# Performance work log

Hardware: AMD Instinct MI355X
Metric: run time of the kernel (lower is better)

## Reference

```python
import jax, jax.numpy as jnp
import numpy as np

EMBED_DIM = 1024
NUM_HEADS = 16
HEAD_DIM = EMBED_DIM // NUM_HEADS
ROPE_BASE = 10000.0


def rotate_half(x):
    d = x.shape[-1] // 2
    x1, x2 = x[..., :d], x[..., d:]
    return jnp.concatenate((-x2, x1), axis=-1)


def setup_inputs() -> dict:
    key = jax.random.key(0)
    k_x, k_wqkv, k_bqkv, k_wo, k_bo = jax.random.split(key, 5)
    C = EMBED_DIM
    x = jax.random.normal(k_x, (4, 2048, C), dtype=jnp.float32)
    s = 1.0 / np.sqrt(C)
    W_qkv = jax.random.uniform(k_wqkv, (C, 3 * C), minval=-s, maxval=s, dtype=jnp.float32)
    b_qkv = jax.random.uniform(k_bqkv, (3 * C,), minval=-s, maxval=s, dtype=jnp.float32)
    W_out = jax.random.uniform(k_wo, (C, C), minval=-s, maxval=s, dtype=jnp.float32)
    b_out = jax.random.uniform(k_bo, (C,), minval=-s, maxval=s, dtype=jnp.float32)
    return {"x": x, "W_qkv": W_qkv, "b_qkv": b_qkv, "W_out": W_out, "b_out": b_out}


def reference(x, W_qkv, b_qkv, W_out, b_out):
    B, T, C = x.shape
    H, Dh = NUM_HEADS, HEAD_DIM
    # fused QKV projection: [B,T,3C] -> [3,B,H,T,Dh]
    qkv = (x @ W_qkv + b_qkv).reshape(B, T, 3, H, Dh).transpose(2, 0, 3, 1, 4)
    q, k, v = qkv[0], qkv[1], qkv[2]
    # rotary embedding: freqs [T, Dh/2] -> emb [T, Dh]
    inv_freq = 1.0 / (ROPE_BASE ** (jnp.arange(0, Dh, 2, dtype=jnp.float32) / Dh))
    freqs = jnp.arange(T, dtype=jnp.float32)[:, None] * inv_freq[None, :]
    emb = jnp.concatenate((freqs, freqs), axis=-1)  # [T, Dh], broadcasts over B,H
    cos, sin = jnp.cos(emb), jnp.sin(emb)
    q = q * cos + rotate_half(q) * sin
    k = k * cos + rotate_half(k) * sin
    # full (non-causal) attention, manual softmax
    scale = 1.0 / np.sqrt(Dh)
    attn = jax.nn.softmax(jnp.einsum("bhqd,bhkd->bhqk", q, k) * scale, axis=-1)
    out = jnp.einsum("bhqk,bhkd->bhqd", attn, v)  # [B,H,T,Dh]
    out = out.transpose(0, 2, 1, 3).reshape(B, T, C)
    return out @ W_out + b_out
```

## Files before the change

kernel.cpp:

```cpp
#include <hip/hip_runtime.h>
#include <math.h>

#define T_SEQ 2048
#define CDIM  1024
#define NH    16
#define DHD   64
#define BATCH 4
#define MROWS (BATCH * T_SEQ)
#define BHN   (BATCH * NH)

typedef _Float16 f16;
typedef __attribute__((ext_vector_type(8))) _Float16 f16x8;
typedef __attribute__((ext_vector_type(4))) _Float16 f16x4;
typedef __attribute__((ext_vector_type(4))) float f32x4;

__device__ __forceinline__ void gl_lds16(const f16* g, f16* l) {
    __builtin_amdgcn_global_load_lds(
        (const __attribute__((address_space(1))) void*)(g),
        (__attribute__((address_space(3))) void*)(l),
        16, 0, 0);
}

__global__ void rope_tables_kernel(float* __restrict__ ctab, float* __restrict__ stab)
{
    int idx = blockIdx.x * 256 + threadIdx.x;
    int t = idx >> 5, i = idx & 31;
    double inv = pow(10000.0, -(double)(2 * i) / 64.0);
    double a = (double)t * inv;
    ctab[idx] = (float)cos(a);
    stab[idx] = (float)sin(a);
}

__global__ __launch_bounds__(256) void xcvt_kernel(
    const float* __restrict__ X, f16* __restrict__ Xf)
{
    int idx = blockIdx.x * 256 + threadIdx.x;
    const float4* src = (const float4*)X + (size_t)idx * 2;
    float4 a = src[0], b = src[1];
    f16x8 o;
    o[0] = (f16)a.x; o[1] = (f16)a.y; o[2] = (f16)a.z; o[3] = (f16)a.w;
    o[4] = (f16)b.x; o[5] = (f16)b.y; o[6] = (f16)b.z; o[7] = (f16)b.w;
    *((f16x8*)Xf + idx) = o;
}

__global__ __launch_bounds__(64) void wcvt_kernel(
    const float* __restrict__ W, f16* __restrict__ Wt, int N)
{
    int lane = threadIdx.x;
    int k0 = blockIdx.x * 8;
    int n = blockIdx.y * 64 + lane;
    f16x8 o;
#pragma unroll
    for (int j = 0; j < 8; j++) o[j] = (f16)W[(size_t)(k0 + j) * N + n];
    *(f16x8*)(Wt + (size_t)n * CDIM + k0) = o;
}

#define GEMM_MAINLOOP(Aimg, Bimg, M0, N0)                                         \
    __shared__ f16 As[128][32], Bs[128][32];                                      \
    const int tid = threadIdx.x, wave = tid >> 6, lane = tid & 63;                \
    const int l16 = lane & 15, quad = lane >> 4;                                  \
    const int wm = wave >> 1, wn = wave & 1;                                      \
    f32x4 acc[4][4];                                                              \
    _Pragma("unroll") for (int i = 0; i < 4; i++)                                 \
        _Pragma("unroll") for (int j = 0; j < 4; j++)                             \
            acc[i][j] = (f32x4){0.f, 0.f, 0.f, 0.f};                              \
    const f16* sbase = (wave < 2) ? (Aimg) : (Bimg);                              \
    f16* lbase = ((wave < 2) ? &As[0][0] : &Bs[0][0]) + (wave & 1) * 2048;        \
    const size_t srow0 = ((wave < 2) ? (size_t)(M0) : (size_t)(N0)) + (wave & 1) * 64; \
    const int srow = lane >> 2, schunk = (lane & 3) << 3;                         \
    for (int k0 = 0; k0 < CDIM; k0 += 32) {                                       \
        _Pragma("unroll") for (int it = 0; it < 4; it++)                          \
            gl_lds16(sbase + (srow0 + it * 16 + srow) * CDIM + k0 + schunk,       \
                     lbase + it * 512);                                           \
        __syncthreads();                                                          \
        f16x8 fa[4], fb[4];                                                       \
        _Pragma("unroll") for (int mi = 0; mi < 4; mi++)                          \
            fa[mi] = *(const f16x8*)&As[wm * 64 + mi * 16 + l16][quad * 8];       \
        _Pragma("unroll") for (int ni = 0; ni < 4; ni++)                          \
            fb[ni] = *(const f16x8*)&Bs[wn * 64 + ni * 16 + l16][quad * 8];       \
        _Pragma("unroll") for (int mi = 0; mi < 4; mi++)                          \
            _Pragma("unroll") for (int ni = 0; ni < 4; ni++)                      \
                acc[mi][ni] = __builtin_amdgcn_mfma_f32_16x16x32_f16(             \
                    fa[mi], fb[ni], acc[mi][ni], 0, 0, 0);                        \
        __syncthreads();                                                          \
    }

__global__ __launch_bounds__(256) void qkv_gemm_kernel(
    const f16* __restrict__ Xf, const f16* __restrict__ Wt,
    const float* __restrict__ bias,
    const float* __restrict__ ctab, const float* __restrict__ stab,
    f16* __restrict__ qf, f16* __restrict__ kf, f16* __restrict__ vf)
{
    const int m0 = blockIdx.x * 128;
    const int n0 = blockIdx.y * 128;
    GEMM_MAINLOOP(Xf, Wt, m0, n0)

    const int ncol0 = n0 + wn * 64;
    const int w = ncol0 >> 10;
    const int h = (ncol0 >> 6) & 15;
    const int b = m0 >> 11;
    const int trow0 = (m0 & 2047) + wm * 64 + quad * 4;
    float bia[4];
#pragma unroll
    for (int ni = 0; ni < 4; ni++) bia[ni] = bias[ncol0 + ni * 16 + l16];

    if (w < 2) {
        f16* oq = w ? kf : qf;
        const float sc = w ? 1.0f : 0.125f;
#pragma unroll
        for (int mi = 0; mi < 4; mi++) {
#pragma unroll
            for (int i = 0; i < 4; i++) {
                int t = trow0 + mi * 16 + i;
                size_t rowoff = ((size_t)(b * NH + h) * T_SEQ + t) * DHD;
#pragma unroll
                for (int np = 0; np < 2; np++) {
                    int d = np * 16 + l16;
                    float v0 = acc[mi][np][i] + bia[np];
                    float v1 = acc[mi][np + 2][i] + bia[np + 2];
                    float c = ctab[(t << 5) + d];
                    float s = stab[(t << 5) + d];
                    oq[rowoff + d]      = (f16)((v0 * c - v1 * s) * sc);
                    oq[rowoff + d + 32] = (f16)((v1 * c + v0 * s) * sc);
                }
            }
        }
    } else {
#pragma unroll
        for (int mi = 0; mi < 4; mi++) {
#pragma unroll
            for (int i = 0; i < 4; i++) {
                int t = trow0 + mi * 16 + i;
                size_t rowoff = ((size_t)(b * NH + h) * T_SEQ + t) * DHD;
#pragma unroll
                for (int ni = 0; ni < 4; ni++)
                    vf[rowoff + ni * 16 + l16] = (f16)(acc[mi][ni][i] + bia[ni]);
            }
        }
    }
}

__global__ __launch_bounds__(256) void vt_kernel(
    const f16* __restrict__ vf, f16* __restrict__ vt)
{
    __shared__ f16 Ls[64][72];
    const int tid = threadIdx.x;
    const int tb = blockIdx.x;
    const int bh = blockIdx.y;
#pragma unroll
    for (int p = 0; p < 2; p++) {
        int idx = tid + p * 256;
        int r = idx >> 3, c8 = (idx & 7) << 3;
        *(f16x8*)&Ls[r][c8] =
            *(const f16x8*)(vf + ((size_t)bh * T_SEQ + tb * 64 + r) * DHD + c8);
    }
    __syncthreads();
#pragma unroll
    for (int p = 0; p < 2; p++) {
        int idx = tid + p * 256;
        int d = idx >> 3, t8 = (idx & 7) << 3;
        f16x8 o;
#pragma unroll
        for (int j = 0; j < 8; j++) o[j] = Ls[t8 + j][d];
        *(f16x8*)(vt + ((size_t)bh * DHD + d) * T_SEQ + (size_t)tb * 64 + t8) = o;
    }
}

__global__ __launch_bounds__(256, 2) void attn_kernel(
    const f16* __restrict__ qf, const f16* __restrict__ kf,
    const f16* __restrict__ vt, f16* __restrict__ ab)
{
    __shared__ f16 Kb[2][64][72];
    __shared__ f16 Vb[2][64][72];
    __shared__ f16 Pb[4][64][40];
    __shared__ float Lb[4][64];

    const int tid  = threadIdx.x;
    const int wave = tid >> 6, lane = tid & 63;
    const int l16  = lane & 15, quad = lane >> 4;
    const int qt = blockIdx.x;
    const int bh = blockIdx.y;
    const int q0 = qt * 256 + wave * 64;

    const f16* kbase = kf + (size_t)bh * T_SEQ * DHD;
    const f16* vbase = vt + (size_t)bh * DHD * T_SEQ;

    f16x8 qfr[4][2];
#pragma unroll
    for (int qs = 0; qs < 4; qs++) {
        const f16* qrow = qf + ((size_t)bh * T_SEQ + q0 + qs * 16 + l16) * DHD;
        qfr[qs][0] = *(const f16x8*)(qrow + quad * 8);
        qfr[qs][1] = *(const f16x8*)(qrow + 32 + quad * 8);
    }

    f32x4 o[4][4];
#pragma unroll
    for (int qs = 0; qs < 4; qs++)
#pragma unroll
        for (int dt = 0; dt < 4; dt++) o[qs][dt] = (f32x4){0.f, 0.f, 0.f, 0.f};
    float lp[4] = {0.f, 0.f, 0.f, 0.f};

    const int srow = tid >> 3;
    const int scol = (tid & 7) << 3;

    f16x8 kreg[2], vreg[2];
#pragma unroll
    for (int r = 0; r < 2; r++) {
        kreg[r] = *(const f16x8*)(kbase + (size_t)(srow + r * 32) * DHD + scol);
        vreg[r] = *(const f16x8*)(vbase + (size_t)(srow + r * 32) * T_SEQ + scol);
    }
#pragma unroll
    for (int r = 0; r < 2; r++) {
        *(f16x8*)&Kb[0][srow + r * 32][scol] = kreg[r];
        *(f16x8*)&Vb[0][srow + r * 32][scol] = vreg[r];
    }
    __syncthreads();

    for (int kt = 0; kt < 32; kt++) {
        const int buf = kt & 1;
        if (kt < 31) {
#pragma unroll
            for (int r = 0; r < 2; r++) {
                kreg[r] = *(const f16x8*)(kbase + (size_t)((kt + 1) * 64 + srow + r * 32) * DHD + scol);
                vreg[r] = *(const f16x8*)(vbase + (size_t)(srow + r * 32) * T_SEQ + (kt + 1) * 64 + scol);
            }
        }

#pragma unroll
        for (int half = 0; half < 2; half++) {
            f32x4 sc[2][4];
#pragma unroll
            for (int k2 = 0; k2 < 2; k2++)
#pragma unroll
                for (int qs = 0; qs < 4; qs++) sc[k2][qs] = (f32x4){0.f, 0.f, 0.f, 0.f};
#pragma unroll
            for (int k2 = 0; k2 < 2; k2++) {
                const int keyt = half * 2 + k2;
#pragma unroll
                for (int ks = 0; ks < 2; ks++) {
                    f16x8 kfr = *(const f16x8*)&Kb[buf][keyt * 16 + l16][ks * 32 + quad * 8];
#pragma unroll
                    for (int qs = 0; qs < 4; qs++)
                        sc[k2][qs] = __builtin_amdgcn_mfma_f32_16x16x32_f16(
                            kfr, qfr[qs][ks], sc[k2][qs], 0, 0, 0);
                }
            }
#pragma unroll
            for (int k2 = 0; k2 < 2; k2++) {
#pragma unroll
                for (int qs = 0; qs < 4; qs++) {
                    f16x4 pv;
#pragma unroll
                    for (int i = 0; i < 4; i++) {
                        float p = __expf(sc[k2][qs][i]);
                        lp[qs] += p;
                        pv[i] = (f16)p;
                    }
                    *(f16x4*)&Pb[wave][qs * 16 + l16][k2 * 16 + quad * 4] = pv;
                }
            }
            f16x8 pfr[4];
#pragma unroll
            for (int qs = 0; qs < 4; qs++)
                pfr[qs] = *(const f16x8*)&Pb[wave][qs * 16 + l16][quad * 8];
#pragma unroll
            for (int dt = 0; dt < 4; dt++) {
                f16x8 vfr = *(const f16x8*)&Vb[buf][dt * 16 + l16][half * 32 + quad * 8];
#pragma unroll
                for (int qs = 0; qs < 4; qs++)
                    o[qs][dt] = __builtin_amdgcn_mfma_f32_16x16x32_f16(
                        pfr[qs], vfr, o[qs][dt], 0, 0, 0);
            }
        }

        if (kt < 31) {
#pragma unroll
            for (int r = 0; r < 2; r++) {
                *(f16x8*)&Kb[buf ^ 1][srow + r * 32][scol] = kreg[r];
                *(f16x8*)&Vb[buf ^ 1][srow + r * 32][scol] = vreg[r];
            }
        }
        __syncthreads();
    }

#pragma unroll
    for (int qs = 0; qs < 4; qs++) {
        float l = lp[qs];
        l += __shfl_xor(l, 16);
        l += __shfl_xor(l, 32);
        Lb[wave][qs * 16 + l16] = 1.f / l;
    }

    const int b = bh >> 4, h = bh & 15;
#pragma unroll
    for (int qs = 0; qs < 4; qs++) {
        f32x4 iv = *(const f32x4*)&Lb[wave][qs * 16 + quad * 4];
#pragma unroll
        for (int i = 0; i < 4; i++) {
            int m = b * T_SEQ + qt * 256 + wave * 64 + qs * 16 + quad * 4 + i;
#pragma unroll
            for (int dt = 0; dt < 4; dt++)
                ab[(size_t)m * CDIM + h * 64 + dt * 16 + l16] = (f16)(o[qs][dt][i] * iv[i]);
        }
    }
}

__global__ __launch_bounds__(256) void out_gemm_kernel(
    const f16* __restrict__ Ab, const f16* __restrict__ Wt,
    const float* __restrict__ bias, float* __restrict__ out)
{
    const int m0 = blockIdx.x * 128;
    const int n0 = blockIdx.y * 128;
    GEMM_MAINLOOP(Ab, Wt, m0, n0)

    const int ncol0 = n0 + wn * 64;
    float bia[4];
#pragma unroll
    for (int ni = 0; ni < 4; ni++) bia[ni] = bias[ncol0 + ni * 16 + l16];
#pragma unroll
    for (int mi = 0; mi < 4; mi++) {
#pragma unroll
        for (int i = 0; i < 4; i++) {
            int m = m0 + wm * 64 + mi * 16 + quad * 4 + i;
#pragma unroll
            for (int ni = 0; ni < 4; ni++)
                out[(size_t)m * CDIM + ncol0 + ni * 16 + l16] = acc[mi][ni][i] + bia[ni];
        }
    }
}

extern "C" void kernel_launch(void* const* d_in, const int* in_sizes, int n_in,
                              void* d_out, int out_size, void* d_ws, size_t ws_size,
                              hipStream_t stream)
{
    const float* x    = (const float*)d_in[0];
    const float* Wqkv = (const float*)d_in[1];
    const float* bqkv = (const float*)d_in[2];
    const float* Wout = (const float*)d_in[3];
    const float* bout = (const float*)d_in[4];
    float* out = (float*)d_out;

    const size_t XSZ  = (size_t)MROWS * CDIM;
    const size_t WQSZ = (size_t)3072 * CDIM;
    const size_t WOSZ = (size_t)CDIM * CDIM;
    const size_t QSZ  = (size_t)BHN * T_SEQ * DHD;

    char* p = (char*)d_ws;
    f16* Xf  = (f16*)p; p += XSZ * 2;
    f16* Wqt = (f16*)p; p += WQSZ * 2;
    f16* Wot = (f16*)p; p += WOSZ * 2;
    f16* qf  = (f16*)p; p += QSZ * 2;
    f16* kf  = (f16*)p; p += QSZ * 2;
    f16* vf  = (f16*)p; p += QSZ * 2;
    f16* vtb = (f16*)p; p += QSZ * 2;
    f16* ab  = (f16*)p; p += QSZ * 2;
    float* ctab = (float*)p; p += T_SEQ * 32 * 4;
    float* stab = (float*)p; p += T_SEQ * 32 * 4;

    rope_tables_kernel<<<256, 256, 0, stream>>>(ctab, stab);
    xcvt_kernel<<<(int)(XSZ / 8 / 256), 256, 0, stream>>>(x, Xf);
    wcvt_kernel<<<dim3(128, 48), 64, 0, stream>>>(Wqkv, Wqt, 3072);
    wcvt_kernel<<<dim3(128, 16), 64, 0, stream>>>(Wout, Wot, 1024);
    qkv_gemm_kernel<<<dim3(64, 24), 256, 0, stream>>>(
        Xf, Wqt, bqkv, ctab, stab, qf, kf, vf);
    vt_kernel<<<dim3(32, BHN), 256, 0, stream>>>(vf, vtb);
    attn_kernel<<<dim3(8, BHN), 256, 0, stream>>>(qf, kf, vtb, ab);
    out_gemm_kernel<<<dim3(64, 8), 256, 0, stream>>>(ab, Wot, bout, out);
}
```

Measured before the change: 308.6 us.

## Shrink attention tiles, swizzle LDS, use exp2 and MFMA row sums

The attention kernel drops to 32 queries per wave (128 per block) and doubles the grid so more blocks fit per CU at launch bounds of 4. The K/V/P LDS tiles lose their padding and use XOR swizzling instead to avoid bank conflicts. The scale log2(e)/8 is folded into Q so softmax can use the hardware exp2, with packed f16 conversion. Row sums are computed by an MFMA against a ones vector instead of scalar adds and shuffles, and block indices are swizzled to group blocks sharing the same head. Smaller query tiles mean each block reloads K/V for fewer queries, which raises global/L2 traffic.

After: 300.2 us. 1.03x faster.

```diff
diff --git a/kernel.cpp b/kernel.cpp
--- a/kernel.cpp
+++ b/kernel.cpp
@@ -12,7 +12,22 @@
 typedef _Float16 f16;
 typedef __attribute__((ext_vector_type(8))) _Float16 f16x8;
 typedef __attribute__((ext_vector_type(4))) _Float16 f16x4;
+typedef __attribute__((ext_vector_type(2))) _Float16 f16x2;
+typedef __attribute__((ext_vector_type(2))) __fp16 fp16x2;
 typedef __attribute__((ext_vector_type(4))) float f32x4;
+
+__device__ __forceinline__ float fast_exp2(float x) {
+#if __has_builtin(__builtin_amdgcn_exp2f)
+    return __builtin_amdgcn_exp2f(x);
+#else
+    return exp2f(x);
+#endif
+}
+
+__device__ __forceinline__ f16x2 cvt_pk_f16(float a, float b) {
+    fp16x2 r = __builtin_amdgcn_cvt_pkrtz(a, b);
+    return __builtin_bit_cast(f16x2, r);
+}
 
 __device__ __forceinline__ void gl_lds16(const f16* g, f16* l) {
     __builtin_amdgcn_global_load_lds(
@@ -106,7 +121,7 @@
 
     if (w < 2) {
         f16* oq = w ? kf : qf;
-        const float sc = w ? 1.0f : 0.125f;
+        const float sc = w ? 1.0f : 0.18033688011112042f;
 #pragma unroll
         for (int mi = 0; mi < 4; mi++) {
 #pragma unroll
@@ -166,42 +181,51 @@
     }
 }
 
-__global__ __launch_bounds__(256, 2) void attn_kernel(
+__global__ __launch_bounds__(256, 4) void attn_kernel(
     const f16* __restrict__ qf, const f16* __restrict__ kf,
     const f16* __restrict__ vt, f16* __restrict__ ab)
 {
-    __shared__ f16 Kb[2][64][72];
-    __shared__ f16 Vb[2][64][72];
-    __shared__ f16 Pb[4][64][40];
-    __shared__ float Lb[4][64];
+    __shared__ f16 Kb[2][64][64];
+    __shared__ f16 Vb[2][64][64];
+    __shared__ f16 Pb[4][32][32];
 
     const int tid  = threadIdx.x;
     const int wave = tid >> 6, lane = tid & 63;
     const int l16  = lane & 15, quad = lane >> 4;
-    const int qt = blockIdx.x;
-    const int bh = blockIdx.y;
-    const int q0 = qt * 256 + wave * 64;
+
+    const int flat = blockIdx.x + (blockIdx.y << 4);
+    const int swz  = (flat & 7) * 128 + (flat >> 3);
+    const int qt = swz & 15;
+    const int bh = swz >> 4;
+    const int q0 = qt * 128 + wave * 32;
 
     const f16* kbase = kf + (size_t)bh * T_SEQ * DHD;
     const f16* vbase = vt + (size_t)bh * DHD * T_SEQ;
 
-    f16x8 qfr[4][2];
-#pragma unroll
-    for (int qs = 0; qs < 4; qs++) {
+    f16x8 qfr[2][2];
+#pragma unroll
+    for (int qs = 0; qs < 2; qs++) {
         const f16* qrow = qf + ((size_t)bh * T_SEQ + q0 + qs * 16 + l16) * DHD;
         qfr[qs][0] = *(const f16x8*)(qrow + quad * 8);
         qfr[qs][1] = *(const f16x8*)(qrow + 32 + quad * 8);
     }
 
-    f32x4 o[4][4];
-#pragma unroll
-    for (int qs = 0; qs < 4; qs++)
+    f32x4 o[2][4];
+    f32x4 lacc[2];
+#pragma unroll
+    for (int qs = 0; qs < 2; qs++) {
+        lacc[qs] = (f32x4){0.f, 0.f, 0.f, 0.f};
 #pragma unroll
         for (int dt = 0; dt < 4; dt++) o[qs][dt] = (f32x4){0.f, 0.f, 0.f, 0.f};
-    float lp[4] = {0.f, 0.f, 0.f, 0.f};
+    }
+    f16x8 ones;
+#pragma unroll
+    for (int j = 0; j < 8; j++) ones[j] = (f16)1.0f;
 
     const int srow = tid >> 3;
-    const int scol = (tid & 7) << 3;
+    const int scw  = tid & 7;
+    const int scol = scw << 3;
+    const int swzc = (scw ^ (srow & 7)) << 3;
 
     f16x8 kreg[2], vreg[2];
 #pragma unroll
@@ -211,8 +235,8 @@
     }
 #pragma unroll
     for (int r = 0; r < 2; r++) {
-        *(f16x8*)&Kb[0][srow + r * 32][scol] = kreg[r];
-        *(f16x8*)&Vb[0][srow + r * 32][scol] = vreg[r];
+        *(f16x8*)&Kb[0][srow + r * 32][swzc] = kreg[r];
+        *(f16x8*)&Vb[0][srow + r * 32][swzc] = vreg[r];
     }
     __syncthreads();
 
@@ -228,19 +252,20 @@
 
 #pragma unroll
         for (int half = 0; half < 2; half++) {
-            f32x4 sc[2][4];
+            f32x4 sc[2][2];
 #pragma unroll
             for (int k2 = 0; k2 < 2; k2++)
 #pragma unroll
-                for (int qs = 0; qs < 4; qs++) sc[k2][qs] = (f32x4){0.f, 0.f, 0.f, 0.f};
+                for (int qs = 0; qs < 2; qs++) sc[k2][qs] = (f32x4){0.f, 0.f, 0.f, 0.f};
 #pragma unroll
             for (int k2 = 0; k2 < 2; k2++) {
                 const int keyt = half * 2 + k2;
 #pragma unroll
                 for (int ks = 0; ks < 2; ks++) {
-                    f16x8 kfr = *(const f16x8*)&Kb[buf][keyt * 16 + l16][ks * 32 + quad * 8];
-#pragma unroll
-                    for (int qs = 0; qs < 4; qs++)
+                    const int kc = ((ks * 4 + quad) ^ (l16 & 7)) << 3;
+                    f16x8 kfr = *(const f16x8*)&Kb[buf][keyt * 16 + l16][kc];
+#pragma unroll
+                    for (int qs = 0; qs < 2; qs++)
                         sc[k2][qs] = __builtin_amdgcn_mfma_f32_16x16x32_f16(
                             kfr, qfr[qs][ks], sc[k2][qs], 0, 0, 0);
                 }
@@ -248,26 +273,33 @@
 #pragma unroll
             for (int k2 = 0; k2 < 2; k2++) {
 #pragma unroll
-                for (int qs = 0; qs < 4; qs++) {
+                for (int qs = 0; qs < 2; qs++) {
+                    f16x2 pa = cvt_pk_f16(
+                        fast_exp2(sc[k2][qs][0]), fast_exp2(sc[k2][qs][1]));
+                    f16x2 pb = cvt_pk_f16(
+                        fast_exp2(sc[k2][qs][2]), fast_exp2(sc[k2][qs][3]));
                     f16x4 pv;
-#pragma unroll
-                    for (int i = 0; i < 4; i++) {
-                        float p = __expf(sc[k2][qs][i]);
-                        lp[qs] += p;
-                        pv[i] = (f16)p;
-                    }
-                    *(f16x4*)&Pb[wave][qs * 16 + l16][k2 * 16 + quad * 4] = pv;
+                    ((f16x2*)&pv)[0] = pa;
+                    ((f16x2*)&pv)[1] = pb;
+                    const int pc = (((k2 * 2 + (quad >> 1)) ^ (l16 & 3)) << 3)
+                                 + ((quad & 1) << 2);
+                    *(f16x4*)&Pb[wave][qs * 16 + l16][pc] = pv;
                 }
             }
-            f16x8 pfr[4];
-#pragma unroll
-            for (int qs = 0; qs < 4; qs++)
-                pfr[qs] = *(const f16x8*)&Pb[wave][qs * 16 + l16][quad * 8];
+            f16x8 pfr[2];
+            const int prc = (quad ^ (l16 & 3)) << 3;
+#pragma unroll
+            for (int qs = 0; qs < 2; qs++) {
+                pfr[qs] = *(const f16x8*)&Pb[wave][qs * 16 + l16][prc];
+                lacc[qs] = __builtin_amdgcn_mfma_f32_16x16x32_f16(
+                    pfr[qs], ones, lacc[qs], 0, 0, 0);
+            }
 #pragma unroll
             for (int dt = 0; dt < 4; dt++) {
-                f16x8 vfr = *(const f16x8*)&Vb[buf][dt * 16 + l16][half * 32 + quad * 8];
-#pragma unroll
-                for (int qs = 0; qs < 4; qs++)
+                const int vc = ((half * 4 + quad) ^ (l16 & 7)) << 3;
+                f16x8 vfr = *(const f16x8*)&Vb[buf][dt * 16 + l16][vc];
+#pragma unroll
+                for (int qs = 0; qs < 2; qs++)
                     o[qs][dt] = __builtin_amdgcn_mfma_f32_16x16x32_f16(
                         pfr[qs], vfr, o[qs][dt], 0, 0, 0);
             }
@@ -276,31 +308,23 @@
         if (kt < 31) {
 #pragma unroll
             for (int r = 0; r < 2; r++) {
-                *(f16x8*)&Kb[buf ^ 1][srow + r * 32][scol] = kreg[r];
-                *(f16x8*)&Vb[buf ^ 1][srow + r * 32][scol] = vreg[r];
+                *(f16x8*)&Kb[buf ^ 1][srow + r * 32][swzc] = kreg[r];
+                *(f16x8*)&Vb[buf ^ 1][srow + r * 32][swzc] = vreg[r];
             }
         }
         __syncthreads();
     }
 
-#pragma unroll
-    for (int qs = 0; qs < 4; qs++) {
-        float l = lp[qs];
-        l += __shfl_xor(l, 16);
-        l += __shfl_xor(l, 32);
-        Lb[wave][qs * 16 + l16] = 1.f / l;
-    }
-
     const int b = bh >> 4, h = bh & 15;
 #pragma unroll
-    for (int qs = 0; qs < 4; qs++) {
-        f32x4 iv = *(const f32x4*)&Lb[wave][qs * 16 + quad * 4];
+    for (int qs = 0; qs < 2; qs++) {
 #pragma unroll
         for (int i = 0; i < 4; i++) {
-            int m = b * T_SEQ + qt * 256 + wave * 64 + qs * 16 + quad * 4 + i;
+            float iv = 1.f / lacc[qs][i];
+            int m = b * T_SEQ + qt * 128 + wave * 32 + qs * 16 + quad * 4 + i;
 #pragma unroll
             for (int dt = 0; dt < 4; dt++)
-                ab[(size_t)m * CDIM + h * 64 + dt * 16 + l16] = (f16)(o[qs][dt][i] * iv[i]);
+                ab[(size_t)m * CDIM + h * 64 + dt * 16 + l16] = (f16)(o[qs][dt][i] * iv);
         }
     }
 }
@@ -364,6 +388,6 @@
     qkv_gemm_kernel<<<dim3(64, 24), 256, 0, stream>>>(
         Xf, Wqt, bqkv, ctab, stab, qf, kf, vf);
     vt_kernel<<<dim3(32, BHN), 256, 0, stream>>>(vf, vtb);
-    attn_kernel<<<dim3(8, BHN), 256, 0, stream>>>(qf, kf, vtb, ab);
+    attn_kernel<<<dim3(16, BHN), 256, 0, stream>>>(qf, kf, vtb, ab);
     out_gemm_kernel<<<dim3(64, 8), 256, 0, stream>>>(ab, Wot, bout, out);
 }
```
